# Kernel optimization log

Measured on AMD Instinct MI355X. Metric: run time of the kernel, lower is better.

Reference implementation:

```python
import jax, jax.numpy as jnp
import numpy as np

H = 64  # hidden size

def lstm_layer(x, h0, c0, Wih, Whh, bih, bhh):
    # x: [B,T,D]; Wih: [4H,D]; Whh: [4H,H]; gate order i,f,g,o (PyTorch)
    xp = jnp.einsum('btd,gd->btg', x, Wih) + bih  # precompute input projections [B,T,4H]
    def step(carry, xt):
        h, c = carry
        gates = xt + h @ Whh.T + bhh
        i, f, g, o = jnp.split(gates, 4, axis=-1)
        c = jax.nn.sigmoid(f) * c + jax.nn.sigmoid(i) * jnp.tanh(g)
        h = jax.nn.sigmoid(o) * jnp.tanh(c)
        return (h, c), h
    (_, _), ys = jax.lax.scan(step, (h0, c0), jnp.swapaxes(xp, 0, 1))  # scan over T
    return jnp.swapaxes(ys, 0, 1)  # [B,T,H]

def setup_inputs() -> dict:
    key = jax.random.key(0)
    ks = jax.random.split(key, 12)
    B, T = 256, 2048
    s = 0.1
    return {
        'input': jax.random.normal(ks[0], (B, T), jnp.float32),
        'h0': jnp.zeros((2, B, H), jnp.float32),
        'c0': jnp.zeros((2, B, H), jnp.float32),
        'Wih0': jax.random.normal(ks[1], (4 * H, 1), jnp.float32) * s,
        'Whh0': jax.random.normal(ks[2], (4 * H, H), jnp.float32) * s,
        'bih0': jax.random.normal(ks[3], (4 * H,), jnp.float32) * s,
        'bhh0': jax.random.normal(ks[4], (4 * H,), jnp.float32) * s,
        'Wih1': jax.random.normal(ks[5], (4 * H, H), jnp.float32) * s,
        'Whh1': jax.random.normal(ks[6], (4 * H, H), jnp.float32) * s,
        'bih1': jax.random.normal(ks[7], (4 * H,), jnp.float32) * s,
        'bhh1': jax.random.normal(ks[8], (4 * H,), jnp.float32) * s,
        'Wlin': jax.random.normal(ks[9], (1, H), jnp.float32) * s,
        'blin': jax.random.normal(ks[10], (1,), jnp.float32) * s,
    }

def reference(input, h0, c0, Wih0, Whh0, bih0, bhh0, Wih1, Whh1, bih1, bhh1, Wlin, blin):
    x = input[..., None]  # [B,T,1]
    y0 = lstm_layer(x, h0[0], c0[0], Wih0, Whh0, bih0, bhh0)
    y1 = lstm_layer(y0, h0[1], c0[1], Wih1, Whh1, bih1, bhh1)
    pred = jnp.einsum('bth,oh->bto', y1, Wlin) + blin  # [B,T,1]
    return pred[..., 0]
```

## Files before the change

kernel.cpp:

```cpp
#include <hip/hip_runtime.h>

#define HD 64
#define KP 16
#define NS 32
#define L2E 1.4426950408889634f

typedef _Float16 v2h __attribute__((ext_vector_type(2)));
typedef _Float16 h8  __attribute__((ext_vector_type(8)));

__device__ __forceinline__ float fexp2(float x) { return __builtin_amdgcn_exp2f(x); }
__device__ __forceinline__ float frcp(float x)  { return __builtin_amdgcn_rcpf(x); }
__device__ __forceinline__ float ftanh_fast(float x) {
    return 1.f - 2.f * frcp(fexp2(2.f * L2E * x) + 1.f);
}
__device__ __forceinline__ float fsig(float x) {
    return frcp(fexp2(-L2E * x) + 1.f);
}

#if __has_builtin(__builtin_amdgcn_fdot2)
__device__ __forceinline__ float FDOT2(v2h a, v2h b, float c) {
    return __builtin_amdgcn_fdot2(a, b, c, false);
}
#else
__device__ __forceinline__ float FDOT2(v2h a, v2h b, float c) {
    return fmaf((float)a.x, (float)b.x, fmaf((float)a.y, (float)b.y, c));
}
#endif

#define DECL32(P) \
    v2h P##_0,P##_1,P##_2,P##_3,P##_4,P##_5,P##_6,P##_7, \
        P##_8,P##_9,P##_10,P##_11,P##_12,P##_13,P##_14,P##_15, \
        P##_16,P##_17,P##_18,P##_19,P##_20,P##_21,P##_22,P##_23, \
        P##_24,P##_25,P##_26,P##_27,P##_28,P##_29,P##_30,P##_31

#define CVT2(v) v2h{(_Float16)v.x, (_Float16)v.y}
#define CVT2H(v) v2h{(_Float16)v.z, (_Float16)v.w}

#define LOAD32(W, r, P) do { \
    const float4* wp_ = (const float4*)((W) + (size_t)(r) * HD); \
    float4 v_; \
    v_=wp_[0];  P##_0 =CVT2(v_); P##_1 =CVT2H(v_); \
    v_=wp_[1];  P##_2 =CVT2(v_); P##_3 =CVT2H(v_); \
    v_=wp_[2];  P##_4 =CVT2(v_); P##_5 =CVT2H(v_); \
    v_=wp_[3];  P##_6 =CVT2(v_); P##_7 =CVT2H(v_); \
    v_=wp_[4];  P##_8 =CVT2(v_); P##_9 =CVT2H(v_); \
    v_=wp_[5];  P##_10=CVT2(v_); P##_11=CVT2H(v_); \
    v_=wp_[6];  P##_12=CVT2(v_); P##_13=CVT2H(v_); \
    v_=wp_[7];  P##_14=CVT2(v_); P##_15=CVT2H(v_); \
    v_=wp_[8];  P##_16=CVT2(v_); P##_17=CVT2H(v_); \
    v_=wp_[9];  P##_18=CVT2(v_); P##_19=CVT2H(v_); \
    v_=wp_[10]; P##_20=CVT2(v_); P##_21=CVT2H(v_); \
    v_=wp_[11]; P##_22=CVT2(v_); P##_23=CVT2H(v_); \
    v_=wp_[12]; P##_24=CVT2(v_); P##_25=CVT2H(v_); \
    v_=wp_[13]; P##_26=CVT2(v_); P##_27=CVT2H(v_); \
    v_=wp_[14]; P##_28=CVT2(v_); P##_29=CVT2H(v_); \
    v_=wp_[15]; P##_30=CVT2(v_); P##_31=CVT2H(v_); \
} while (0)

#define DOTG(P, i0, i1, i2, i3, A0, A1) \
    A0 = FDOT2(P##_##i0, p0_, A0); A1 = FDOT2(P##_##i1, p1_, A1); \
    A0 = FDOT2(P##_##i2, p2_, A0); A1 = FDOT2(P##_##i3, p3_, A1);

#define DOTBLK4(HP, q, i0, i1, i2, i3) \
    { h8 hv_ = (HP)[q]; \
      v2h p0_={hv_[0],hv_[1]}, p1_={hv_[2],hv_[3]}; \
      v2h p2_={hv_[4],hv_[5]}, p3_={hv_[6],hv_[7]}; \
      DOTG(wgA, i0,i1,i2,i3, a00,a01) DOTG(wgB, i0,i1,i2,i3, a10,a11) \
      DOTG(wgC, i0,i1,i2,i3, a20,a21) DOTG(wgD, i0,i1,i2,i3, a30,a31) }

#define DOT4N(HP) \
    DOTBLK4(HP,0, 0,1,2,3)     DOTBLK4(HP,1, 4,5,6,7) \
    DOTBLK4(HP,2, 8,9,10,11)   DOTBLK4(HP,3, 12,13,14,15) \
    DOTBLK4(HP,4, 16,17,18,19) DOTBLK4(HP,5, 20,21,22,23) \
    DOTBLK4(HP,6, 24,25,26,27) DOTBLK4(HP,7, 28,29,30,31)

__global__ __launch_bounds__(256) __attribute__((amdgpu_waves_per_eu(1, 1)))
void lstm2_kernel(const float* __restrict__ x,
                  const float* __restrict__ h0in,
                  const float* __restrict__ c0in,
                  const float* __restrict__ Wih0,
                  const float* __restrict__ Whh0,
                  const float* __restrict__ bih0,
                  const float* __restrict__ bhh0,
                  const float* __restrict__ Wih1,
                  const float* __restrict__ Whh1,
                  const float* __restrict__ bih1,
                  const float* __restrict__ bhh1,
                  const float* __restrict__ Wlin,
                  const float* __restrict__ blin,
                  float* __restrict__ out,
                  int B, int T)
{
    const int b    = blockIdx.x;
    const int tid  = threadIdx.x;
    const int wave = tid >> 6;
    const int lane = tid & 63;

    __shared__ __align__(16) _Float16 h0ring[NS][HD];
    __shared__ __align__(16) _Float16 h1ring[NS][HD];
    __shared__ __align__(16) float    h1f32[NS][HD + 4];
    __shared__ __align__(16) float    xpring[NS][4][HD];
    __shared__ float ldspad[8192];

    {
        _Float16* z0 = &h0ring[0][0];
        for (int i = tid; i < NS * HD; i += 256) z0[i] = (_Float16)0.f;
        _Float16* z1 = &h1ring[0][0];
        for (int i = tid; i < NS * HD; i += 256) z1[i] = (_Float16)0.f;
        float* z2 = &h1f32[0][0];
        for (int i = tid; i < NS * (HD + 4); i += 256) z2[i] = 0.f;
        float* z3 = &xpring[0][0][0];
        for (int i = tid; i < NS * 4 * HD; i += 256) z3[i] = 0.f;
        ldspad[tid] = 0.f;
    }
    __syncthreads();
    { float pv = ldspad[tid]; asm volatile("" :: "v"(pv)); }

    const int nphase = (T + KP - 1) / KP + 3;

    if (wave == 0) {
        DECL32(wgA); DECL32(wgB); DECL32(wgC); DECL32(wgD);
        LOAD32(Whh0, lane,        wgA);
        LOAD32(Whh0, 64 + lane,   wgB);
        LOAD32(Whh0, 128 + lane,  wgC);
        LOAD32(Whh0, 192 + lane,  wgD);
        const float b0 = bih0[lane]       + bhh0[lane];
        const float b1 = bih0[64 + lane]  + bhh0[64 + lane];
        const float b2 = bih0[128 + lane] + bhh0[128 + lane];
        const float b3 = bih0[192 + lane] + bhh0[192 + lane];
        const float wx0 = Wih0[lane];       const float wx1 = Wih0[64 + lane];
        const float wx2 = Wih0[128 + lane]; const float wx3 = Wih0[192 + lane];
        float cst = c0in[b * HD + lane];
        h0ring[NS - 1][lane] = (_Float16)h0in[b * HD + lane];
        const float* xrow = x + (size_t)b * T;
        __syncthreads();

        for (int p = 0; p < nphase; ++p) {
            const int t0 = p * KP;
            if (t0 < T) {
                #pragma unroll 1
                for (int k = 0; k < KP; ++k) {
                    const int t = t0 + k;
                    if (t >= T) break;
                    const float xv = xrow[t];
                    const h8* hp = (const h8*)h0ring[(t + NS - 1) & (NS - 1)];
                    float a00 = b0, a01 = 0.f, a10 = b1, a11 = 0.f;
                    float a20 = b2, a21 = 0.f, a30 = b3, a31 = 0.f;
                    DOT4N(hp);
                    const float ai = fmaf(wx0, xv, a00 + a01);
                    const float af = fmaf(wx1, xv, a10 + a11);
                    const float ag = fmaf(wx2, xv, a20 + a21);
                    const float ao = fmaf(wx3, xv, a30 + a31);
                    const float iv = fsig(ai), fv = fsig(af);
                    const float gv = ftanh_fast(ag), ov = fsig(ao);
                    cst = fmaf(fv, cst, iv * gv);
                    const float h = ov * ftanh_fast(cst);
                    h0ring[t & (NS - 1)][lane] = (_Float16)h;
                }
            }
            __syncthreads();
        }
    } else if (wave == 1) {
        DECL32(wgA); DECL32(wgB); DECL32(wgC); DECL32(wgD);
        LOAD32(Whh1, lane,        wgA);
        LOAD32(Whh1, 64 + lane,   wgB);
        LOAD32(Whh1, 128 + lane,  wgC);
        LOAD32(Whh1, 192 + lane,  wgD);
        float cst = c0in[B * HD + b * HD + lane];
        h1ring[NS - 1][lane] = (_Float16)h0in[B * HD + b * HD + lane];
        __syncthreads();

        for (int p = 0; p < nphase; ++p) {
            const int t0 = (p - 2) * KP;
            if (p >= 2 && t0 < T) {
                #pragma unroll 1
                for (int k = 0; k < KP; ++k) {
                    const int t = t0 + k;
                    if (t >= T) break;
                    const int s = t & (NS - 1);
                    const float x0 = xpring[s][0][lane];
                    const float x1 = xpring[s][1][lane];
                    const float x2 = xpring[s][2][lane];
                    const float x3 = xpring[s][3][lane];
                    const h8* hp = (const h8*)h1ring[(t + NS - 1) & (NS - 1)];
                    float a00 = 0.f, a01 = 0.f, a10 = 0.f, a11 = 0.f;
                    float a20 = 0.f, a21 = 0.f, a30 = 0.f, a31 = 0.f;
                    DOT4N(hp);
                    const float ai = x0 + a00 + a01;
                    const float af = x1 + a10 + a11;
                    const float ag = x2 + a20 + a21;
                    const float ao = x3 + a30 + a31;
                    const float iv = fsig(ai), fv = fsig(af);
                    const float gv = ftanh_fast(ag), ov = fsig(ao);
                    cst = fmaf(fv, cst, iv * gv);
                    const float h = ov * ftanh_fast(cst);
                    h1ring[s][lane] = (_Float16)h;
                    h1f32[s][lane]  = h;
                }
            }
            __syncthreads();
        }
    } else if (wave == 2) {
        DECL32(wgA); DECL32(wgB); DECL32(wgC); DECL32(wgD);
        LOAD32(Wih1, lane,        wgA);
        LOAD32(Wih1, 64 + lane,   wgB);
        LOAD32(Wih1, 128 + lane,  wgC);
        LOAD32(Wih1, 192 + lane,  wgD);
        const float b0 = bih1[lane]       + bhh1[lane];
        const float b1 = bih1[64 + lane]  + bhh1[64 + lane];
        const float b2 = bih1[128 + lane] + bhh1[128 + lane];
        const float b3 = bih1[192 + lane] + bhh1[192 + lane];
        __syncthreads();

        for (int p = 0; p < nphase; ++p) {
            const int t0 = (p - 1) * KP;
            if (p >= 1 && t0 < T) {
                #pragma unroll 1
                for (int k = 0; k < KP; ++k) {
                    const int t = t0 + k;
                    if (t >= T) break;
                    const int s = t & (NS - 1);
                    const h8* hp = (const h8*)h0ring[s];
                    float a00 = b0, a01 = 0.f, a10 = b1, a11 = 0.f;
                    float a20 = b2, a21 = 0.f, a30 = b3, a31 = 0.f;
                    DOT4N(hp);
                    xpring[s][0][lane] = a00 + a01;
                    xpring[s][1][lane] = a10 + a11;
                    xpring[s][2][lane] = a20 + a21;
                    xpring[s][3][lane] = a30 + a31;
                }
            }
            __syncthreads();
        }
    } else {
        const float blin0 = blin[0];
        __syncthreads();

        for (int p = 0; p < nphase; ++p) {
            const int t0 = (p - 3) * KP;
            if (p >= 3 && t0 < T && lane < KP) {
                const int t = t0 + lane;
                if (t < T) {
                    const float4* hv4 = (const float4*)h1f32[t & (NS - 1)];
                    const float4* wp  = (const float4*)Wlin;
                    float acc = blin0;
                    #pragma unroll
                    for (int q = 0; q < 16; ++q) {
                        const float4 hv = hv4[q];
                        const float4 wv = wp[q];
                        acc = fmaf(wv.x, hv.x, acc);
                        acc = fmaf(wv.y, hv.y, acc);
                        acc = fmaf(wv.z, hv.z, acc);
                        acc = fmaf(wv.w, hv.w, acc);
                    }
                    out[(size_t)b * T + t] = acc;
                }
            }
            __syncthreads();
        }
    }
}

extern "C" void kernel_launch(void* const* d_in, const int* in_sizes, int n_in,
                              void* d_out, int out_size, void* d_ws, size_t ws_size,
                              hipStream_t stream)
{
    const float* x    = (const float*)d_in[0];
    const float* h0   = (const float*)d_in[1];
    const float* c0   = (const float*)d_in[2];
    const float* Wih0 = (const float*)d_in[3];
    const float* Whh0 = (const float*)d_in[4];
    const float* bih0 = (const float*)d_in[5];
    const float* bhh0 = (const float*)d_in[6];
    const float* Wih1 = (const float*)d_in[7];
    const float* Whh1 = (const float*)d_in[8];
    const float* bih1 = (const float*)d_in[9];
    const float* bhh1 = (const float*)d_in[10];
    const float* Wlin = (const float*)d_in[11];
    const float* blin = (const float*)d_in[12];
    float* out = (float*)d_out;

    const int B = in_sizes[1] / (2 * HD);
    const int T = in_sizes[0] / B;

    lstm2_kernel<<<dim3(B), dim3(256), 0, stream>>>(
        x, h0, c0, Wih0, Whh0, bih0, bhh0,
        Wih1, Whh1, bih1, bhh1, Wlin, blin, out, B, T);
}
```

Measured before the change: 991.3 us.

## Move LSTM recurrent weights from registers into shared memory

Weights Whh0, Whh1 and Wih1 are now converted to fp16 and stored in LDS in a lane-interleaved v4h layout, instead of each wave holding 128 packed registers of weights. This drops the waves_per_eu(1,1) attribute and the LDS padding array that was used to force one block per CU, so more blocks can share a CU. The cost is extra LDS reads on every timestep's serial critical path, added to the existing h-vector loads.

```diff
diff --git a/kernel.cpp b/kernel.cpp
--- a/kernel.cpp
+++ b/kernel.cpp
@@ -6,6 +6,7 @@
 #define L2E 1.4426950408889634f
 
 typedef _Float16 v2h __attribute__((ext_vector_type(2)));
+typedef _Float16 v4h __attribute__((ext_vector_type(4)));
 typedef _Float16 h8  __attribute__((ext_vector_type(8)));
 
 __device__ __forceinline__ float fexp2(float x) { return __builtin_amdgcn_exp2f(x); }
@@ -27,54 +28,36 @@
 }
 #endif
 
-#define DECL32(P) \
-    v2h P##_0,P##_1,P##_2,P##_3,P##_4,P##_5,P##_6,P##_7, \
-        P##_8,P##_9,P##_10,P##_11,P##_12,P##_13,P##_14,P##_15, \
-        P##_16,P##_17,P##_18,P##_19,P##_20,P##_21,P##_22,P##_23, \
-        P##_24,P##_25,P##_26,P##_27,P##_28,P##_29,P##_30,P##_31
-
-#define CVT2(v) v2h{(_Float16)v.x, (_Float16)v.y}
-#define CVT2H(v) v2h{(_Float16)v.z, (_Float16)v.w}
-
-#define LOAD32(W, r, P) do { \
-    const float4* wp_ = (const float4*)((W) + (size_t)(r) * HD); \
-    float4 v_; \
-    v_=wp_[0];  P##_0 =CVT2(v_); P##_1 =CVT2H(v_); \
-    v_=wp_[1];  P##_2 =CVT2(v_); P##_3 =CVT2H(v_); \
-    v_=wp_[2];  P##_4 =CVT2(v_); P##_5 =CVT2H(v_); \
-    v_=wp_[3];  P##_6 =CVT2(v_); P##_7 =CVT2H(v_); \
-    v_=wp_[4];  P##_8 =CVT2(v_); P##_9 =CVT2H(v_); \
-    v_=wp_[5];  P##_10=CVT2(v_); P##_11=CVT2H(v_); \
-    v_=wp_[6];  P##_12=CVT2(v_); P##_13=CVT2H(v_); \
-    v_=wp_[7];  P##_14=CVT2(v_); P##_15=CVT2H(v_); \
-    v_=wp_[8];  P##_16=CVT2(v_); P##_17=CVT2H(v_); \
-    v_=wp_[9];  P##_18=CVT2(v_); P##_19=CVT2H(v_); \
-    v_=wp_[10]; P##_20=CVT2(v_); P##_21=CVT2H(v_); \
-    v_=wp_[11]; P##_22=CVT2(v_); P##_23=CVT2H(v_); \
-    v_=wp_[12]; P##_24=CVT2(v_); P##_25=CVT2H(v_); \
-    v_=wp_[13]; P##_26=CVT2(v_); P##_27=CVT2H(v_); \
-    v_=wp_[14]; P##_28=CVT2(v_); P##_29=CVT2H(v_); \
-    v_=wp_[15]; P##_30=CVT2(v_); P##_31=CVT2H(v_); \
-} while (0)
-
-#define DOTG(P, i0, i1, i2, i3, A0, A1) \
-    A0 = FDOT2(P##_##i0, p0_, A0); A1 = FDOT2(P##_##i1, p1_, A1); \
-    A0 = FDOT2(P##_##i2, p2_, A0); A1 = FDOT2(P##_##i3, p3_, A1);
-
-#define DOTBLK4(HP, q, i0, i1, i2, i3) \
-    { h8 hv_ = (HP)[q]; \
-      v2h p0_={hv_[0],hv_[1]}, p1_={hv_[2],hv_[3]}; \
-      v2h p2_={hv_[4],hv_[5]}, p3_={hv_[6],hv_[7]}; \
-      DOTG(wgA, i0,i1,i2,i3, a00,a01) DOTG(wgB, i0,i1,i2,i3, a10,a11) \
-      DOTG(wgC, i0,i1,i2,i3, a20,a21) DOTG(wgD, i0,i1,i2,i3, a30,a31) }
-
-#define DOT4N(HP) \
-    DOTBLK4(HP,0, 0,1,2,3)     DOTBLK4(HP,1, 4,5,6,7) \
-    DOTBLK4(HP,2, 8,9,10,11)   DOTBLK4(HP,3, 12,13,14,15) \
-    DOTBLK4(HP,4, 16,17,18,19) DOTBLK4(HP,5, 20,21,22,23) \
-    DOTBLK4(HP,6, 24,25,26,27) DOTBLK4(HP,7, 28,29,30,31)
-
-__global__ __launch_bounds__(256) __attribute__((amdgpu_waves_per_eu(1, 1)))
+
+#define DOTLDS4(M, HP) do { \
+    _Pragma("unroll") \
+    for (int q = 0; q < 8; ++q) { \
+        h8 hv_ = (HP)[q]; \
+        v2h p0_={hv_[0],hv_[1]}, p1_={hv_[2],hv_[3]}; \
+        v2h p2_={hv_[4],hv_[5]}, p3_={hv_[6],hv_[7]}; \
+        v4h wA0 = wlds[M][0][2*q][lane], wA1 = wlds[M][0][2*q+1][lane]; \
+        v4h wB0 = wlds[M][1][2*q][lane], wB1 = wlds[M][1][2*q+1][lane]; \
+        v4h wC0 = wlds[M][2][2*q][lane], wC1 = wlds[M][2][2*q+1][lane]; \
+        v4h wD0 = wlds[M][3][2*q][lane], wD1 = wlds[M][3][2*q+1][lane]; \
+        a00 = FDOT2(v2h{wA0[0],wA0[1]}, p0_, a00); \
+        a01 = FDOT2(v2h{wA0[2],wA0[3]}, p1_, a01); \
+        a00 = FDOT2(v2h{wA1[0],wA1[1]}, p2_, a00); \
+        a01 = FDOT2(v2h{wA1[2],wA1[3]}, p3_, a01); \
+        a10 = FDOT2(v2h{wB0[0],wB0[1]}, p0_, a10); \
+        a11 = FDOT2(v2h{wB0[2],wB0[3]}, p1_, a11); \
+        a10 = FDOT2(v2h{wB1[0],wB1[1]}, p2_, a10); \
+        a11 = FDOT2(v2h{wB1[2],wB1[3]}, p3_, a11); \
+        a20 = FDOT2(v2h{wC0[0],wC0[1]}, p0_, a20); \
+        a21 = FDOT2(v2h{wC0[2],wC0[3]}, p1_, a21); \
+        a20 = FDOT2(v2h{wC1[0],wC1[1]}, p2_, a20); \
+        a21 = FDOT2(v2h{wC1[2],wC1[3]}, p3_, a21); \
+        a30 = FDOT2(v2h{wD0[0],wD0[1]}, p0_, a30); \
+        a31 = FDOT2(v2h{wD0[2],wD0[3]}, p1_, a31); \
+        a30 = FDOT2(v2h{wD1[0],wD1[1]}, p2_, a30); \
+        a31 = FDOT2(v2h{wD1[2],wD1[3]}, p3_, a31); \
+    } } while (0)
+
+__global__ __launch_bounds__(256)
 void lstm2_kernel(const float* __restrict__ x,
                   const float* __restrict__ h0in,
                   const float* __restrict__ c0in,
@@ -93,14 +76,14 @@
 {
     const int b    = blockIdx.x;
     const int tid  = threadIdx.x;
-    const int wave = tid >> 6;
+    const int wave = __builtin_amdgcn_readfirstlane(tid >> 6);
     const int lane = tid & 63;
 
+    __shared__ __align__(16) v4h wlds[3][4][16][HD];
     __shared__ __align__(16) _Float16 h0ring[NS][HD];
     __shared__ __align__(16) _Float16 h1ring[NS][HD];
     __shared__ __align__(16) float    h1f32[NS][HD + 4];
     __shared__ __align__(16) float    xpring[NS][4][HD];
-    __shared__ float ldspad[8192];
 
     {
         _Float16* z0 = &h0ring[0][0];
@@ -111,19 +94,28 @@
         for (int i = tid; i < NS * (HD + 4); i += 256) z2[i] = 0.f;
         float* z3 = &xpring[0][0][0];
         for (int i = tid; i < NS * 4 * HD; i += 256) z3[i] = 0.f;
-        ldspad[tid] = 0.f;
+    }
+
+    {
+        const int r = tid;
+        const int g = r >> 6, j = r & 63;
+        const float* srcs[3] = { Whh0, Whh1, Wih1 };
+        #pragma unroll
+        for (int m = 0; m < 3; ++m) {
+            const float4* s4 = (const float4*)(srcs[m] + (size_t)r * HD);
+            #pragma unroll
+            for (int qq = 0; qq < 16; ++qq) {
+                float4 v = s4[qq];
+                wlds[m][g][qq][j] =
+                    v4h{(_Float16)v.x, (_Float16)v.y, (_Float16)v.z, (_Float16)v.w};
+            }
+        }
     }
     __syncthreads();
-    { float pv = ldspad[tid]; asm volatile("" :: "v"(pv)); }
 
     const int nphase = (T + KP - 1) / KP + 3;
 
     if (wave == 0) {
-        DECL32(wgA); DECL32(wgB); DECL32(wgC); DECL32(wgD);
-        LOAD32(Whh0, lane,        wgA);
-        LOAD32(Whh0, 64 + lane,   wgB);
-        LOAD32(Whh0, 128 + lane,  wgC);
-        LOAD32(Whh0, 192 + lane,  wgD);
         const float b0 = bih0[lane]       + bhh0[lane];
         const float b1 = bih0[64 + lane]  + bhh0[64 + lane];
         const float b2 = bih0[128 + lane] + bhh0[128 + lane];
@@ -146,7 +138,7 @@
                     const h8* hp = (const h8*)h0ring[(t + NS - 1) & (NS - 1)];
                     float a00 = b0, a01 = 0.f, a10 = b1, a11 = 0.f;
                     float a20 = b2, a21 = 0.f, a30 = b3, a31 = 0.f;
-                    DOT4N(hp);
+                    DOTLDS4(0, hp);
                     const float ai = fmaf(wx0, xv, a00 + a01);
                     const float af = fmaf(wx1, xv, a10 + a11);
                     const float ag = fmaf(wx2, xv, a20 + a21);
@@ -161,11 +153,6 @@
             __syncthreads();
         }
     } else if (wave == 1) {
-        DECL32(wgA); DECL32(wgB); DECL32(wgC); DECL32(wgD);
-        LOAD32(Whh1, lane,        wgA);
-        LOAD32(Whh1, 64 + lane,   wgB);
-        LOAD32(Whh1, 128 + lane,  wgC);
-        LOAD32(Whh1, 192 + lane,  wgD);
         float cst = c0in[B * HD + b * HD + lane];
         h1ring[NS - 1][lane] = (_Float16)h0in[B * HD + b * HD + lane];
         __syncthreads();
@@ -185,7 +172,7 @@
                     const h8* hp = (const h8*)h1ring[(t + NS - 1) & (NS - 1)];
                     float a00 = 0.f, a01 = 0.f, a10 = 0.f, a11 = 0.f;
                     float a20 = 0.f, a21 = 0.f, a30 = 0.f, a31 = 0.f;
-                    DOT4N(hp);
+                    DOTLDS4(1, hp);
                     const float ai = x0 + a00 + a01;
                     const float af = x1 + a10 + a11;
                     const float ag = x2 + a20 + a21;
@@ -201,11 +188,6 @@
             __syncthreads();
         }
     } else if (wave == 2) {
-        DECL32(wgA); DECL32(wgB); DECL32(wgC); DECL32(wgD);
-        LOAD32(Wih1, lane,        wgA);
-        LOAD32(Wih1, 64 + lane,   wgB);
-        LOAD32(Wih1, 128 + lane,  wgC);
-        LOAD32(Wih1, 192 + lane,  wgD);
         const float b0 = bih1[lane]       + bhh1[lane];
         const float b1 = bih1[64 + lane]  + bhh1[64 + lane];
         const float b2 = bih1[128 + lane] + bhh1[128 + lane];
@@ -223,7 +205,7 @@
                     const h8* hp = (const h8*)h0ring[s];
                     float a00 = b0, a01 = 0.f, a10 = b1, a11 = 0.f;
                     float a20 = b2, a21 = 0.f, a30 = b3, a31 = 0.f;
-                    DOT4N(hp);
+                    DOTLDS4(2, hp);
                     xpring[s][0][lane] = a00 + a01;
                     xpring[s][1][lane] = a10 + a11;
                     xpring[s][2][lane] = a20 + a21;
```

After: 1.619 ms. +63.3%, slower.
